# Optimization experiments

Hardware: AMD Instinct MI355X
Metric: run time of the kernel (lower is better)

The kernel has to match this reference:

```python
import jax, jax.numpy as jnp
import numpy as np

B, T, D, H, QK = 4, 2048, 1024, 16, 64
MAX_WAVELENGTH = 10000


def apply_rope(x, positions):
    # x: [B, T, H, d]; positions: [B, T] int
    d = x.shape[-1]
    fraction = 2 * jnp.arange(0, d // 2, dtype=jnp.int32) / d
    timescale = MAX_WAVELENGTH ** fraction  # [d/2]
    sinusoid = positions[..., None] / timescale[None, :]  # [B, T, d/2]
    sinusoid = sinusoid[..., None, :]  # [B, T, 1, d/2]
    sin, cos = jnp.sin(sinusoid), jnp.cos(sinusoid)
    x1, x2 = jnp.split(x, 2, axis=-1)
    return jnp.concatenate([x1 * cos - x2 * sin, x2 * cos + x1 * sin], axis=-1).astype(x.dtype)


def rms_norm(x, scale):
    var = jnp.mean(jnp.square(x), axis=-1, keepdims=True)
    return x * jax.lax.rsqrt(var + 1e-6) * (1 + scale)


def setup_inputs() -> dict:
    key = jax.random.key(0)
    ks = jax.random.split(key, 12)
    s = 0.02
    pos = jnp.broadcast_to(jnp.arange(T, dtype=jnp.int32), (B, T))
    causal = jnp.tril(jnp.ones((T, T), dtype=bool))[None, None]  # [1,1,T,T]
    return {
        "q": jax.random.normal(ks[0], (B, T, D), jnp.float32),
        "kv": jax.random.normal(ks[1], (B, T, D), jnp.float32),
        "mask": jnp.broadcast_to(causal, (B, 1, T, T)),
        "q_positions": pos,
        "kv_positions": pos,
        "Wq": jax.random.normal(ks[2], (D, H * QK), jnp.float32) * s,
        "bq": jnp.zeros((H * QK,), jnp.float32),
        "Wk": jax.random.normal(ks[3], (D, H * QK), jnp.float32) * s,
        "bk": jnp.zeros((H * QK,), jnp.float32),
        "Wv": jax.random.normal(ks[4], (D, H * QK), jnp.float32) * s,
        "bv": jnp.zeros((H * QK,), jnp.float32),
        "q_scale": jnp.zeros((QK,), jnp.float32),
        "k_scale": jnp.zeros((QK,), jnp.float32),
        "head_scale": jnp.zeros((1, H, 1), jnp.float32),
        "Wo": jax.random.normal(ks[5], (H * QK, D), jnp.float32) * s,
        "bo": jnp.zeros((D,), jnp.float32),
    }


def reference(q, kv, mask, q_positions, kv_positions, Wq, bq, Wk, bk, Wv, bv,
              q_scale, k_scale, head_scale, Wo, bo):
    qh = (q @ Wq + bq).reshape(B, T, H, QK)
    kh = (kv @ Wk + bk).reshape(B, T, H, QK)
    vh = (kv @ Wv + bv).reshape(B, T, H, QK)
    # qk layer norm (RMSNorm with (1+scale))
    qh = rms_norm(qh, q_scale)
    kh = rms_norm(kh, k_scale)
    # RoPE
    qh = apply_rope(qh, q_positions)
    kh = apply_rope(kh, kv_positions)
    # attention
    logits = jnp.einsum('bthd,bThd->bhtT', qh, kh) / np.sqrt(QK).astype(q.dtype)
    logits = jnp.where(mask, logits, jnp.finfo(logits.dtype).min)
    weights = jax.nn.softmax(logits, axis=-1)
    weights = jnp.where(mask, weights, 0)
    attn = jnp.einsum('bhtT,bThd->bthd', weights, vh)
    attn = attn * (1 + head_scale)  # [1,H,1] broadcasts over (t,h,d)
    return attn.reshape(B, T, H * QK) @ Wo + bo
```

## Files before the change

kernel.cpp:

```cpp
#include <hip/hip_runtime.h>
#include <math.h>

#define BB 4
#define TT 2048
#define DD 1024
#define HH 16
#define QKD 64
#define MM (BB*TT)
#define NN 1024
#define KK 1024

#define BKQ 32
#define NTS (KK/BKQ)

typedef unsigned short u16;
typedef __attribute__((ext_vector_type(8))) short short8;
typedef __attribute__((ext_vector_type(4))) float float4v;

__device__ __forceinline__ u16 f2bf(float f) {
    union { float f; unsigned u; } v; v.f = f;
    unsigned r = (v.u + 0x7FFFu + ((v.u >> 16) & 1u)) >> 16;
    return (u16)r;
}

__device__ __forceinline__ unsigned cvt_pk_bf16(float lo, float hi) {
    unsigned r;
    asm("v_cvt_pk_bf16_f32 %0, %1, %2" : "=v"(r) : "v"(lo), "v"(hi));
    return r;
}

typedef __attribute__((address_space(3))) unsigned lds_u32_t;
typedef __attribute__((address_space(1))) const unsigned glb_u32_t;
__device__ __forceinline__ void gl2lds16(const u16* g, u16* l) {
    __builtin_amdgcn_global_load_lds((glb_u32_t*)g, (lds_u32_t*)l, 16, 0, 0);
}

__global__ __launch_bounds__(256) void acast_kernel(
    const float* __restrict__ a, const float* __restrict__ b,
    u16* __restrict__ da, u16* __restrict__ db)
{
    const float* s = blockIdx.y ? b : a;
    u16* d = blockIdx.y ? db : da;
    size_t i = ((size_t)blockIdx.x * 256 + threadIdx.x) * 4;
    float4 v = *(const float4*)&s[i];
    ushort4 o = { f2bf(v.x), f2bf(v.y), f2bf(v.z), f2bf(v.w) };
    *(ushort4*)&d[i] = o;
}

__global__ __launch_bounds__(256) void wt_kernel(
    const float* __restrict__ Wq, const float* __restrict__ Wk,
    const float* __restrict__ Wv, const float* __restrict__ Wo,
    u16* __restrict__ dstbase)
{
    const int z = blockIdx.z;
    const float* src = (z == 0) ? Wq : (z == 1) ? Wk : (z == 2) ? Wv : Wo;
    u16* out = dstbase + (size_t)z * (KK * NN);
    const int bi = blockIdx.y, bj = blockIdx.x;
    __shared__ float tile[64][65];
    const int t = threadIdx.x;
    #pragma unroll
    for (int p = 0; p < 4; p++) {
        int idx = p * 256 + t;
        int r = idx >> 4, c4 = (idx & 15) << 2;
        float4 v = *(const float4*)&src[(size_t)(bi * 64 + r) * NN + bj * 64 + c4];
        tile[r][c4 + 0] = v.x; tile[r][c4 + 1] = v.y;
        tile[r][c4 + 2] = v.z; tile[r][c4 + 3] = v.w;
    }
    __syncthreads();
    #pragma unroll
    for (int p = 0; p < 4; p++) {
        int idx = p * 256 + t;
        int rn = idx >> 4, c4 = (idx & 15) << 2;
        ushort4 o = { f2bf(tile[c4 + 0][rn]), f2bf(tile[c4 + 1][rn]),
                      f2bf(tile[c4 + 2][rn]), f2bf(tile[c4 + 3][rn]) };
        *(ushort4*)&out[(size_t)(bj * 64 + rn) * KK + bi * 64 + c4] = o;
    }
}

__device__ __forceinline__ void gemm256_mainloop(
    const u16* __restrict__ A, const u16* __restrict__ Bt,
    int m0, int n0, u16* __restrict__ sh, float4v (&acc)[8][4])
{
    const int tid = threadIdx.x;
    const int lane = tid & 63;
    const int l15 = lane & 15, lg = lane >> 4;
    const int wave = tid >> 6;
    const int wm = wave >> 2, wn = wave & 3;

    u16* sA = sh;
    u16* sB = sh + 16384;

    const int c0 = tid, c1 = 512 + tid;
    const int r0s = c0 >> 2, g0 = (c0 & 3) ^ (r0s & 3);
    const int r1s = c1 >> 2, g1 = (c1 & 3) ^ (r1s & 3);

    const u16* gA0 = A  + (size_t)(m0 + r0s) * KK + g0 * 8;
    const u16* gA1 = A  + (size_t)(m0 + r1s) * KK + g1 * 8;
    const u16* gB0 = Bt + (size_t)(n0 + r0s) * KK + g0 * 8;
    const u16* gB1 = Bt + (size_t)(n0 + r1s) * KK + g1 * 8;

    auto issue = [&](int buf, int k0) {
        u16* dA = sA + buf * (256 * 32);
        u16* dB = sB + buf * (256 * 32);
        gl2lds16(gA0 + k0, dA + c0 * 8);
        gl2lds16(gA1 + k0, dA + c1 * 8);
        gl2lds16(gB0 + k0, dB + c0 * 8);
        gl2lds16(gB1 + k0, dB + c1 * 8);
    };

    issue(0, 0);
    issue(1, BKQ);
    asm volatile("s_waitcnt vmcnt(4)" ::: "memory");
    __builtin_amdgcn_s_barrier();
    __builtin_amdgcn_sched_barrier(0);

    for (int t = 0; t < NTS; t++) {
        const int buf = t & 1;
        const u16* cA = sA + buf * (256 * 32);
        const u16* cB = sB + buf * (256 * 32);

        short8 af[8], bf[4];
        #pragma unroll
        for (int x = 0; x < 8; x++) {
            int ra = wm * 128 + x * 16 + l15;
            af[x] = *(const short8*)(cA + (ra * 4 + (lg ^ (ra & 3))) * 8);
        }
        #pragma unroll
        for (int x = 0; x < 4; x++) {
            int rb = wn * 64 + x * 16 + l15;
            bf[x] = *(const short8*)(cB + (rb * 4 + (lg ^ (rb & 3))) * 8);
        }
        __builtin_amdgcn_s_setprio(1);
        #pragma unroll
        for (int mi = 0; mi < 8; mi++)
            #pragma unroll
            for (int nj = 0; nj < 4; nj++)
                acc[mi][nj] = __builtin_amdgcn_mfma_f32_16x16x32_bf16(af[mi], bf[nj], acc[mi][nj], 0, 0, 0);
        __builtin_amdgcn_s_setprio(0);

        __builtin_amdgcn_s_barrier();
        if (t + 2 < NTS) {
            issue(buf, (t + 2) * BKQ);
            asm volatile("s_waitcnt vmcnt(4)" ::: "memory");
        } else {
            asm volatile("s_waitcnt vmcnt(0)" ::: "memory");
        }
        __builtin_amdgcn_s_barrier();
        __builtin_amdgcn_sched_barrier(0);
    }
}

__device__ __forceinline__ void xcd_swizzle_4x32(int& m_idx, int& n_idx) {
    const int flat = blockIdx.y * 4 + blockIdx.x;
    const int xcd = flat & 7, q = flat >> 3;
    m_idx = xcd * 4 + (q & 3);
    n_idx = q >> 2;
}

__global__ __launch_bounds__(512) void qkv_gemm(
    const u16* __restrict__ qb, const u16* __restrict__ kvb,
    const u16* __restrict__ Wt,
    const float* __restrict__ bq, const float* __restrict__ bk, const float* __restrict__ bv,
    const int* __restrict__ qpos, const int* __restrict__ kpos,
    const float* __restrict__ q_scale, const float* __restrict__ k_scale,
    u16* __restrict__ qh, u16* __restrict__ kh, u16* __restrict__ vt)
{
    __shared__ __align__(16) u16 sh[32768];

    const int z = blockIdx.z;
    const u16* A        = (z == 0) ? qb : kvb;
    const u16* B        = Wt + (size_t)z * (KK * NN);
    const float* bias   = (z == 0) ? bq : (z == 1) ? bk : bv;
    const float* scl    = (z == 0) ? q_scale : k_scale;
    const int* pos_arr  = (z == 0) ? qpos : kpos;
    u16* dst            = (z == 0) ? qh : (z == 1) ? kh : vt;

    int m_idx, n_idx;
    xcd_swizzle_4x32(m_idx, n_idx);
    const int m0 = m_idx * 256, n0 = n_idx * 256;

    float4v acc[8][4];
    #pragma unroll
    for (int i = 0; i < 8; i++)
        #pragma unroll
        for (int j = 0; j < 4; j++) acc[i][j] = (float4v){0.f, 0.f, 0.f, 0.f};

    gemm256_mainloop(A, B, m0, n0, sh, acc);

    const int tid = threadIdx.x;
    const int lane = tid & 63, wave = tid >> 6;
    const int l15 = lane & 15, lg = lane >> 4;
    const int wm = wave >> 2, wn = wave & 3;

    float bia[4], sc[4];
    #pragma unroll
    for (int nj = 0; nj < 4; nj++) {
        bia[nj] = bias[n0 + wn * 64 + nj * 16 + l15];
        sc[nj]  = 1.0f + scl[nj * 16 + l15];
    }
    float invts[2];
    #pragma unroll
    for (int p = 0; p < 2; p++)
        invts[p] = powf(10000.0f, -(float)(p * 16 + l15) * (1.0f / 32.0f));

    const float QMUL = 0.125f * 1.44269504088896340736f;
    const int bb_ = m0 >> 11;
    const int t0g = m0 & 2047;

    if (z < 2) {
        #pragma unroll
        for (int p = 0; p < 2; p++) {
            __syncthreads();
            if (wm == p) {
                #pragma unroll
                for (int mi = 0; mi < 8; mi++) {
                    #pragma unroll
                    for (int r = 0; r < 4; r++) {
                        const int tl = mi * 16 + lg * 4 + r;
                        const int m = m0 + p * 128 + tl;
                        const int b = m >> 11, t = m & 2047;
                        float v[4];
                        #pragma unroll
                        for (int nj = 0; nj < 4; nj++) v[nj] = acc[mi][nj][r] + bia[nj];

                        float ss = v[0]*v[0] + v[1]*v[1] + v[2]*v[2] + v[3]*v[3];
                        ss += __shfl_xor(ss, 1);
                        ss += __shfl_xor(ss, 2);
                        ss += __shfl_xor(ss, 4);
                        ss += __shfl_xor(ss, 8);
                        float rn = rsqrtf(ss * (1.0f / 64.0f) + 1e-6f);
                        #pragma unroll
                        for (int nj = 0; nj < 4; nj++) v[nj] = v[nj] * rn * sc[nj];

                        const float pos = (float)pos_arr[b * TT + t];
                        #pragma unroll
                        for (int pp = 0; pp < 2; pp++) {
                            float ang = pos * invts[pp];
                            float s = sinf(ang), c = cosf(ang);
                            float x1 = v[pp], x2 = v[pp + 2];
                            v[pp]     = x1 * c - x2 * s;
                            v[pp + 2] = x2 * c + x1 * s;
                        }
                        if (z == 0) {
                            #pragma unroll
                            for (int nj = 0; nj < 4; nj++) v[nj] *= QMUL;
                        }
                        #pragma unroll
                        for (int nj = 0; nj < 4; nj++) {
                            const int dl = wn * 64 + nj * 16 + l15;
                            sh[tl * 256 + (dl ^ ((tl & 7) << 3))] = f2bf(v[nj]);
                        }
                    }
                }
            }
            __syncthreads();
            #pragma unroll
            for (int it = 0; it < 8; it++) {
                int idx = it * 512 + tid;
                int tl  = idx >> 5;
                int c8  = (idx & 31) << 3;
                short8 v8 = *(const short8*)&sh[tl * 256 + (c8 ^ ((tl & 7) << 3))];
                int cg = n0 + c8;
                int hh_ = cg >> 6, dih = cg & 63;
                int t = t0g + p * 128 + tl;
                *(short8*)&dst[((size_t)(bb_ * HH + hh_) * TT + t) * QKD + dih] = v8;
            }
        }
    } else {
        #pragma unroll
        for (int p = 0; p < 2; p++) {
            __syncthreads();
            if (wm == p) {
                #pragma unroll
                for (int mi = 0; mi < 8; mi++) {
                    #pragma unroll
                    for (int r = 0; r < 4; r++) {
                        const int tl = mi * 16 + lg * 4 + r;
                        #pragma unroll
                        for (int nj = 0; nj < 4; nj++) {
                            const int dl = wn * 64 + nj * 16 + l15;
                            sh[dl * 128 + (tl ^ ((dl & 7) << 3))] = f2bf(acc[mi][nj][r] + bia[nj]);
                        }
                    }
                }
            }
            __syncthreads();
            #pragma unroll
            for (int it = 0; it < 8; it++) {
                int idx = it * 512 + tid;
                int dl  = idx >> 4;
                int tc  = (idx & 15) << 3;
                short8 v8 = *(const short8*)&sh[dl * 128 + (tc ^ ((dl & 7) << 3))];
                int dg = n0 + dl;
                int hh_ = dg >> 6, dih = dg & 63;
                *(short8*)&vt[((size_t)(bb_ * HH + hh_) * QKD + dih) * TT + t0g + p * 128 + tc] = v8;
            }
        }
    }
}

__global__ __launch_bounds__(512) void out_gemm(
    const u16* __restrict__ A, const u16* __restrict__ Bt,
    const float* __restrict__ bo, float* __restrict__ out)
{
    __shared__ __align__(16) u16 sh[32768];

    int m_idx, n_idx;
    xcd_swizzle_4x32(m_idx, n_idx);
    const int m0 = m_idx * 256, n0 = n_idx * 256;

    float4v acc[8][4];
    #pragma unroll
    for (int i = 0; i < 8; i++)
        #pragma unroll
        for (int j = 0; j < 4; j++) acc[i][j] = (float4v){0.f, 0.f, 0.f, 0.f};

    gemm256_mainloop(A, Bt, m0, n0, sh, acc);

    const int lane = threadIdx.x & 63, wave = threadIdx.x >> 6;
    const int l15 = lane & 15, lg = lane >> 4;
    const int wm = wave >> 2, wn = wave & 3;

    float bov[4];
    #pragma unroll
    for (int nj = 0; nj < 4; nj++) bov[nj] = bo[n0 + wn * 64 + nj * 16 + l15];

    #pragma unroll
    for (int mi = 0; mi < 8; mi++)
        #pragma unroll
        for (int r = 0; r < 4; r++) {
            const int m = m0 + wm * 128 + mi * 16 + lg * 4 + r;
            float* op = out + (size_t)m * NN + n0 + wn * 64 + l15;
            #pragma unroll
            for (int nj = 0; nj < 4; nj++)
                op[nj * 16] = acc[mi][nj][r] + bov[nj];
        }
}

__global__ __launch_bounds__(256) void attn_mfma(
    const u16* __restrict__ qh, const u16* __restrict__ kh,
    const u16* __restrict__ vt, const float* __restrict__ head_scale,
    u16* __restrict__ out)
{
    __shared__ __align__(16) u16 Ks[2][64 * 64];
    __shared__ __align__(16) u16 Vs[2][64 * 64];
    __shared__ __align__(16) u16 Ps[4][16 * 64];

    const int b = blockIdx.z, h = blockIdx.y;
    const int qta = blockIdx.x;
    const int qtb = 31 - qta;
    const int t0a = qta * 64, t0b = qtb * 64;

    const int tid  = threadIdx.x;
    const int wave = tid >> 6, lane = tid & 63;
    const int l15 = lane & 15, lg = lane >> 4;
    const int l7 = l15 & 7;

    const size_t bh = (size_t)(b * HH + h);
    const u16* qbh  = qh + bh * TT * QKD;
    const u16* kbh  = kh + bh * TT * QKD;
    const u16* vtbh = vt + bh * QKD * TT;

    short8 qfA[2], qfB[2];
    #pragma unroll
    for (int kc = 0; kc < 2; kc++) {
        qfA[kc] = *(const short8*)(qbh + (size_t)(t0a + wave * 16 + l15) * QKD
                                    + kc * 32 + lg * 8);
        qfB[kc] = *(const short8*)(qbh + (size_t)(t0b + wave * 16 + l15) * QKD
                                    + kc * 32 + lg * 8);
    }

    auto stage = [&](int buf, int j0s) {
        #pragma unroll
        for (int rr = 0; rr < 2; rr++) {
            const int c   = rr * 256 + tid;
            const int row = c >> 3;
            const int g   = (c & 7) ^ (row & 7);
            u16* ldsK = &Ks[buf][(rr * 256 + (wave << 6)) * 8];
            u16* ldsV = &Vs[buf][(rr * 256 + (wave << 6)) * 8];
            gl2lds16(kbh  + (size_t)(j0s + row) * QKD + g * 8, ldsK);
            gl2lds16(vtbh + (size_t)row * TT + j0s + g * 8, ldsV);
        }
    };

    float4v oA[4], oB[4];
    #pragma unroll
    for (int nt = 0; nt < 4; nt++) {
        oA[nt] = (float4v){0.f, 0.f, 0.f, 0.f};
        oB[nt] = (float4v){0.f, 0.f, 0.f, 0.f};
    }
    float mA[4] = {-INFINITY, -INFINITY, -INFINITY, -INFINITY};
    float mB[4] = {-INFINITY, -INFINITY, -INFINITY, -INFINITY};
    float lA[4] = {0.f, 0.f, 0.f, 0.f};
    float lB[4] = {0.f, 0.f, 0.f, 0.f};

    auto flash_step = [&](int cur, int jt, int qt_self,
                          short8 (&qf)[2], float4v (&oa)[4],
                          float (&mr)[4], float (&lr)[4]) {
        float4v sarr[4];
        #pragma unroll
        for (int nt = 0; nt < 4; nt++) {
            float4v s = (float4v){0.f, 0.f, 0.f, 0.f};
            #pragma unroll
            for (int kc = 0; kc < 2; kc++) {
                const short8 bfrag = *(const short8*)
                    &Ks[cur][(nt * 16 + l15) * 64 + ((kc * 4 + lg) ^ l7) * 8];
                s = __builtin_amdgcn_mfma_f32_16x16x32_bf16(qf[kc], bfrag, s, 0, 0, 0);
            }
            sarr[nt] = s;
        }

        if (jt == qt_self) {
            const int qbase = qt_self * 64 + wave * 16 + lg * 4;
            #pragma unroll
            for (int nt = 0; nt < 4; nt++) {
                int jkey = jt * 64 + nt * 16 + l15;
                #pragma unroll
                for (int r = 0; r < 4; r++)
                    if (jkey > qbase + r) sarr[nt][r] = -INFINITY;
            }
        }

        float pm[4];
        #pragma unroll
        for (int r = 0; r < 4; r++) {
            float m = fmaxf(fmaxf(sarr[0][r], sarr[1][r]), fmaxf(sarr[2][r], sarr[3][r]));
            m = fmaxf(m, __shfl_xor(m, 1));
            m = fmaxf(m, __shfl_xor(m, 2));
            m = fmaxf(m, __shfl_xor(m, 4));
            m = fmaxf(m, __shfl_xor(m, 8));
            pm[r] = m;
        }
        float grow = fmaxf(fmaxf(pm[0] - mr[0], pm[1] - mr[1]),
                           fmaxf(pm[2] - mr[2], pm[3] - mr[3]));
        if (__any(grow > 8.0f)) {
            #pragma unroll
            for (int r = 0; r < 4; r++) {
                float mn = fmaxf(mr[r], pm[r]);
                float a  = exp2f(mr[r] - mn);
                mr[r] = mn;
                lr[r] *= a;
                #pragma unroll
                for (int nt = 0; nt < 4; nt++) oa[nt][r] *= a;
            }
        }

        u16* pw = Ps[wave];
        float lp[4] = {0.f, 0.f, 0.f, 0.f};
        #pragma unroll
        for (int nt = 0; nt < 4; nt++) {
            float p0 = exp2f(sarr[nt][0] - mr[0]);
            float p1 = exp2f(sarr[nt][1] - mr[1]);
            float p2 = exp2f(sarr[nt][2] - mr[2]);
            float p3 = exp2f(sarr[nt][3] - mr[3]);
            lp[0] += p0; lp[1] += p1; lp[2] += p2; lp[3] += p3;
            unsigned wlo = cvt_pk_bf16(p0, p1);
            unsigned whi = cvt_pk_bf16(p2, p3);
            const int gb = nt * 2 + (l15 >> 3);
            const int r0 = lg * 4;
            pw[(r0 + 0) * 64 + ((gb ^ ((r0 + 0) & 7))) * 8 + l7] = (u16)wlo;
            pw[(r0 + 1) * 64 + ((gb ^ ((r0 + 1) & 7))) * 8 + l7] = (u16)(wlo >> 16);
            pw[(r0 + 2) * 64 + ((gb ^ ((r0 + 2) & 7))) * 8 + l7] = (u16)whi;
            pw[(r0 + 3) * 64 + ((gb ^ ((r0 + 3) & 7))) * 8 + l7] = (u16)(whi >> 16);
        }
        #pragma unroll
        for (int r = 0; r < 4; r++) lr[r] += lp[r];

        short8 pf[2];
        #pragma unroll
        for (int kc = 0; kc < 2; kc++)
            pf[kc] = *(const short8*)&pw[l15 * 64 + ((kc * 4 + lg) ^ l7) * 8];

        #pragma unroll
        for (int nt = 0; nt < 4; nt++) {
            #pragma unroll
            for (int kc = 0; kc < 2; kc++) {
                const short8 vfrag = *(const short8*)
                    &Vs[cur][(nt * 16 + l15) * 64 + ((kc * 4 + lg) ^ l7) * 8];
                oa[nt] = __builtin_amdgcn_mfma_f32_16x16x32_bf16(pf[kc], vfrag, oa[nt], 0, 0, 0);
            }
        }
    };

    stage(0, 0);
    __syncthreads();

    const int njt = qtb + 1;
    for (int jt = 0; jt < njt; jt++) {
        const int cur = jt & 1;
        if (jt + 1 < njt) stage(cur ^ 1, (jt + 1) * 64);

        flash_step(cur, jt, qtb, qfB, oB, mB, lB);
        if (jt <= qta)
            flash_step(cur, jt, qta, qfA, oA, mA, lA);

        __syncthreads();
    }

    const float hs = 1.0f + head_scale[h];
    auto epilogue = [&](int t0, float4v (&oa)[4], float (&lr)[4]) {
        #pragma unroll
        for (int r = 0; r < 4; r++) {
            float l = lr[r];
            l += __shfl_xor(l, 1);
            l += __shfl_xor(l, 2);
            l += __shfl_xor(l, 4);
            l += __shfl_xor(l, 8);
            const int q = t0 + wave * 16 + lg * 4 + r;
            const float f = hs / l;
            u16* op = out + ((size_t)(b * TT + q) * NN) + h * QKD + l15;
            #pragma unroll
            for (int nt = 0; nt < 4; nt++)
                op[nt * 16] = f2bf(oa[nt][r] * f);
        }
    };
    epilogue(t0b, oB, lB);
    epilogue(t0a, oA, lA);
}

extern "C" void kernel_launch(void* const* d_in, const int* in_sizes, int n_in,
                              void* d_out, int out_size, void* d_ws, size_t ws_size,
                              hipStream_t stream)
{
    const float* q          = (const float*)d_in[0];
    const float* kv         = (const float*)d_in[1];
    const int*   qpos       = (const int*)d_in[3];
    const int*   kpos       = (const int*)d_in[4];
    const float* Wq         = (const float*)d_in[5];
    const float* bq         = (const float*)d_in[6];
    const float* Wk         = (const float*)d_in[7];
    const float* bk         = (const float*)d_in[8];
    const float* Wv         = (const float*)d_in[9];
    const float* bv         = (const float*)d_in[10];
    const float* q_scale    = (const float*)d_in[11];
    const float* k_scale    = (const float*)d_in[12];
    const float* head_scale = (const float*)d_in[13];
    const float* Wo         = (const float*)d_in[14];
    const float* bo         = (const float*)d_in[15];
    float* out = (float*)d_out;

    char* ws = (char*)d_ws;
    u16* qb     = (u16*)(ws);
    u16* kvb    = (u16*)(ws + (16u << 20));
    u16* Wt     = (u16*)(ws + (32u << 20));
    u16* qh_b   = (u16*)(ws + (40u << 20));
    u16* kh_b   = (u16*)(ws + (56u << 20));
    u16* vt_b   = (u16*)(ws + (72u << 20));
    u16* attn_b = (u16*)(ws + (88u << 20));

    acast_kernel<<<dim3(MM * DD / (256 * 4), 2), 256, 0, stream>>>(q, kv, qb, kvb);
    wt_kernel<<<dim3(16, 16, 4), 256, 0, stream>>>(Wq, Wk, Wv, Wo, Wt);
    qkv_gemm<<<dim3(NN / 256, MM / 256, 3), 512, 0, stream>>>(
        qb, kvb, Wt, bq, bk, bv, qpos, kpos, q_scale, k_scale, qh_b, kh_b, vt_b);
    attn_mfma<<<dim3(TT / 128, HH, BB), 256, 0, stream>>>(qh_b, kh_b, vt_b, head_scale, attn_b);
    out_gemm<<<dim3(NN / 256, MM / 256), 512, 0, stream>>>(attn_b, Wt + (size_t)3 * KK * NN, bo, out);
}
```

Before: 487.8 us.

## Triple-buffer GEMM main loop with split A-fragment loads and new LDS swizzle

Turns the shared 256x256 GEMM main loop from double to triple buffering: three K-tiles are prefetched and each iteration needs only one barrier pair, with graded vmcnt waits. A-fragment LDS reads are split into two halves interleaved with MFMA groups, and the XOR swizzle now uses (row>>1)&3 to change the bank-conflict pattern. LDS per block grows to 96 KB and launch bounds request 2 blocks per CU, which may raise register pressure or prevent two blocks from co-residing. The aim is to hide global-load latency and LDS-read stalls in both QKV and output projections.

```diff
diff --git a/kernel.cpp b/kernel.cpp
--- a/kernel.cpp
+++ b/kernel.cpp
@@ -87,12 +87,9 @@
     const int wave = tid >> 6;
     const int wm = wave >> 2, wn = wave & 3;
 
-    u16* sA = sh;
-    u16* sB = sh + 16384;
-
     const int c0 = tid, c1 = 512 + tid;
-    const int r0s = c0 >> 2, g0 = (c0 & 3) ^ (r0s & 3);
-    const int r1s = c1 >> 2, g1 = (c1 & 3) ^ (r1s & 3);
+    const int r0s = c0 >> 2, g0 = (c0 & 3) ^ ((r0s >> 1) & 3);
+    const int r1s = c1 >> 2, g1 = (c1 & 3) ^ ((r1s >> 1) & 3);
 
     const u16* gA0 = A  + (size_t)(m0 + r0s) * KK + g0 * 8;
     const u16* gA1 = A  + (size_t)(m0 + r1s) * KK + g1 * 8;
@@ -100,8 +97,8 @@
     const u16* gB1 = Bt + (size_t)(n0 + r1s) * KK + g1 * 8;
 
     auto issue = [&](int buf, int k0) {
-        u16* dA = sA + buf * (256 * 32);
-        u16* dB = sB + buf * (256 * 32);
+        u16* dA = sh + buf * 16384;
+        u16* dB = dA + 8192;
         gl2lds16(gA0 + k0, dA + c0 * 8);
         gl2lds16(gA1 + k0, dA + c1 * 8);
         gl2lds16(gB0 + k0, dB + c0 * 8);
@@ -110,42 +107,55 @@
 
     issue(0, 0);
     issue(1, BKQ);
-    asm volatile("s_waitcnt vmcnt(4)" ::: "memory");
-    __builtin_amdgcn_s_barrier();
-    __builtin_amdgcn_sched_barrier(0);
-
+    issue(2, 2 * BKQ);
+
+    int buf = 0;
     for (int t = 0; t < NTS; t++) {
-        const int buf = t & 1;
-        const u16* cA = sA + buf * (256 * 32);
-        const u16* cB = sB + buf * (256 * 32);
-
-        short8 af[8], bf[4];
-        #pragma unroll
-        for (int x = 0; x < 8; x++) {
-            int ra = wm * 128 + x * 16 + l15;
-            af[x] = *(const short8*)(cA + (ra * 4 + (lg ^ (ra & 3))) * 8);
-        }
+        if (t < NTS - 2)       asm volatile("s_waitcnt vmcnt(8)" ::: "memory");
+        else if (t == NTS - 2) asm volatile("s_waitcnt vmcnt(4)" ::: "memory");
+        else                   asm volatile("s_waitcnt vmcnt(0)" ::: "memory");
+        __builtin_amdgcn_s_barrier();
+        __builtin_amdgcn_sched_barrier(0);
+
+        const u16* cA = sh + buf * 16384;
+        const u16* cB = cA + 8192;
+
+        short8 bf[4];
         #pragma unroll
         for (int x = 0; x < 4; x++) {
             int rb = wn * 64 + x * 16 + l15;
-            bf[x] = *(const short8*)(cB + (rb * 4 + (lg ^ (rb & 3))) * 8);
+            bf[x] = *(const short8*)(cB + (rb * 4 + (lg ^ ((rb >> 1) & 3))) * 8);
+        }
+        short8 afl[4];
+        #pragma unroll
+        for (int x = 0; x < 4; x++) {
+            int ra = wm * 128 + x * 16 + l15;
+            afl[x] = *(const short8*)(cA + (ra * 4 + (lg ^ ((ra >> 1) & 3))) * 8);
         }
         __builtin_amdgcn_s_setprio(1);
         #pragma unroll
-        for (int mi = 0; mi < 8; mi++)
+        for (int mi = 0; mi < 4; mi++)
             #pragma unroll
             for (int nj = 0; nj < 4; nj++)
-                acc[mi][nj] = __builtin_amdgcn_mfma_f32_16x16x32_bf16(af[mi], bf[nj], acc[mi][nj], 0, 0, 0);
+                acc[mi][nj] = __builtin_amdgcn_mfma_f32_16x16x32_bf16(afl[mi], bf[nj], acc[mi][nj], 0, 0, 0);
         __builtin_amdgcn_s_setprio(0);
+        short8 afh[4];
+        #pragma unroll
+        for (int x = 0; x < 4; x++) {
+            int ra = wm * 128 + (4 + x) * 16 + l15;
+            afh[x] = *(const short8*)(cA + (ra * 4 + (lg ^ ((ra >> 1) & 3))) * 8);
+        }
+        __builtin_amdgcn_s_setprio(1);
+        #pragma unroll
+        for (int mi = 0; mi < 4; mi++)
+            #pragma unroll
+            for (int nj = 0; nj < 4; nj++)
+                acc[4 + mi][nj] = __builtin_amdgcn_mfma_f32_16x16x32_bf16(afh[mi], bf[nj], acc[4 + mi][nj], 0, 0, 0);
+        __builtin_amdgcn_s_setprio(0);
 
         __builtin_amdgcn_s_barrier();
-        if (t + 2 < NTS) {
-            issue(buf, (t + 2) * BKQ);
-            asm volatile("s_waitcnt vmcnt(4)" ::: "memory");
-        } else {
-            asm volatile("s_waitcnt vmcnt(0)" ::: "memory");
-        }
-        __builtin_amdgcn_s_barrier();
+        if (t + 3 < NTS) issue(buf, (t + 3) * BKQ);
+        buf = (buf == 2) ? 0 : buf + 1;
         __builtin_amdgcn_sched_barrier(0);
     }
 }
@@ -157,7 +167,7 @@
     n_idx = q >> 2;
 }
 
-__global__ __launch_bounds__(512) void qkv_gemm(
+__global__ __launch_bounds__(512, 2) void qkv_gemm(
     const u16* __restrict__ qb, const u16* __restrict__ kvb,
     const u16* __restrict__ Wt,
     const float* __restrict__ bq, const float* __restrict__ bk, const float* __restrict__ bv,
@@ -165,7 +175,7 @@
     const float* __restrict__ q_scale, const float* __restrict__ k_scale,
     u16* __restrict__ qh, u16* __restrict__ kh, u16* __restrict__ vt)
 {
-    __shared__ __align__(16) u16 sh[32768];
+    __shared__ __align__(16) u16 sh[49152];
 
     const int z = blockIdx.z;
     const u16* A        = (z == 0) ? qb : kvb;
@@ -299,11 +309,11 @@
     }
 }
 
-__global__ __launch_bounds__(512) void out_gemm(
+__global__ __launch_bounds__(512, 2) void out_gemm(
     const u16* __restrict__ A, const u16* __restrict__ Bt,
     const float* __restrict__ bo, float* __restrict__ out)
 {
-    __shared__ __align__(16) u16 sh[32768];
+    __shared__ __align__(16) u16 sh[49152];
 
     int m_idx, n_idx;
     xcd_swizzle_4x32(m_idx, n_idx);
```

Result: no change. 482.3 us (-1.1%).

## Deepen GEMM K-tile to 64 with new LDS swizzle and restructured double buffering

Applied to the files above, without the earlier changes.

The shared 256x256 GEMM mainloop now loads 64-wide K tiles (16 iterations instead of 32). It uses a 3-bit XOR swizzle over eight 16-byte slots per row and a simpler issue-next-then-compute double-buffer loop. LDS per block doubles to 128 KB, and launch bounds request 2 blocks per CU. The aim is to halve barrier and wait overhead per unit of MFMA work. The larger LDS footprint may limit occupancy, and prefetch distance drops from two tiles ahead to one.

```diff
diff --git a/kernel.cpp b/kernel.cpp
--- a/kernel.cpp
+++ b/kernel.cpp
@@ -10,8 +10,8 @@
 #define NN 1024
 #define KK 1024
 
-#define BKQ 32
-#define NTS (KK/BKQ)
+#define BKG 64
+#define NTSG (KK/BKG)
 
 typedef unsigned short u16;
 typedef __attribute__((ext_vector_type(8))) short short8;
@@ -33,6 +33,11 @@
 typedef __attribute__((address_space(1))) const unsigned glb_u32_t;
 __device__ __forceinline__ void gl2lds16(const u16* g, u16* l) {
     __builtin_amdgcn_global_load_lds((glb_u32_t*)g, (lds_u32_t*)l, 16, 0, 0);
+}
+
+__device__ __forceinline__ int swz_slot(int row, int slot) {
+    const int j = (row >> 2) & 3;
+    return slot ^ ((j & 1) | ((j & 2) * 3));
 }
 
 __global__ __launch_bounds__(256) void acast_kernel(
@@ -87,64 +92,64 @@
     const int wave = tid >> 6;
     const int wm = wave >> 2, wn = wave & 3;
 
-    u16* sA = sh;
-    u16* sB = sh + 16384;
-
-    const int c0 = tid, c1 = 512 + tid;
-    const int r0s = c0 >> 2, g0 = (c0 & 3) ^ (r0s & 3);
-    const int r1s = c1 >> 2, g1 = (c1 & 3) ^ (r1s & 3);
-
-    const u16* gA0 = A  + (size_t)(m0 + r0s) * KK + g0 * 8;
-    const u16* gA1 = A  + (size_t)(m0 + r1s) * KK + g1 * 8;
-    const u16* gB0 = Bt + (size_t)(n0 + r0s) * KK + g0 * 8;
-    const u16* gB1 = Bt + (size_t)(n0 + r1s) * KK + g1 * 8;
+    const u16* gA[4]; const u16* gB[4]; int ld_off[4];
+    #pragma unroll
+    for (int i = 0; i < 4; i++) {
+        const int c = tid + i * 512;
+        const int r = c >> 3, sp = c & 7;
+        const int gs = swz_slot(r, sp);
+        gA[i] = A  + (size_t)(m0 + r) * KK + gs * 8;
+        gB[i] = Bt + (size_t)(n0 + r) * KK + gs * 8;
+        ld_off[i] = c * 8;
+    }
 
     auto issue = [&](int buf, int k0) {
-        u16* dA = sA + buf * (256 * 32);
-        u16* dB = sB + buf * (256 * 32);
-        gl2lds16(gA0 + k0, dA + c0 * 8);
-        gl2lds16(gA1 + k0, dA + c1 * 8);
-        gl2lds16(gB0 + k0, dB + c0 * 8);
-        gl2lds16(gB1 + k0, dB + c1 * 8);
+        u16* dA = sh + buf * 32768;
+        u16* dB = dA + 16384;
+        #pragma unroll
+        for (int i = 0; i < 4; i++) gl2lds16(gA[i] + k0, dA + ld_off[i]);
+        #pragma unroll
+        for (int i = 0; i < 4; i++) gl2lds16(gB[i] + k0, dB + ld_off[i]);
     };
 
     issue(0, 0);
-    issue(1, BKQ);
-    asm volatile("s_waitcnt vmcnt(4)" ::: "memory");
-    __builtin_amdgcn_s_barrier();
-    __builtin_amdgcn_sched_barrier(0);
-
-    for (int t = 0; t < NTS; t++) {
+
+    for (int t = 0; t < NTSG; t++) {
         const int buf = t & 1;
-        const u16* cA = sA + buf * (256 * 32);
-        const u16* cB = sB + buf * (256 * 32);
-
-        short8 af[8], bf[4];
-        #pragma unroll
-        for (int x = 0; x < 8; x++) {
-            int ra = wm * 128 + x * 16 + l15;
-            af[x] = *(const short8*)(cA + (ra * 4 + (lg ^ (ra & 3))) * 8);
-        }
-        #pragma unroll
-        for (int x = 0; x < 4; x++) {
-            int rb = wn * 64 + x * 16 + l15;
-            bf[x] = *(const short8*)(cB + (rb * 4 + (lg ^ (rb & 3))) * 8);
-        }
-        __builtin_amdgcn_s_setprio(1);
-        #pragma unroll
-        for (int mi = 0; mi < 8; mi++)
-            #pragma unroll
-            for (int nj = 0; nj < 4; nj++)
-                acc[mi][nj] = __builtin_amdgcn_mfma_f32_16x16x32_bf16(af[mi], bf[nj], acc[mi][nj], 0, 0, 0);
-        __builtin_amdgcn_s_setprio(0);
-
-        __builtin_amdgcn_s_barrier();
-        if (t + 2 < NTS) {
-            issue(buf, (t + 2) * BKQ);
-            asm volatile("s_waitcnt vmcnt(4)" ::: "memory");
+        if (t + 1 < NTSG) {
+            issue(buf ^ 1, (t + 1) * BKG);
+            asm volatile("s_waitcnt vmcnt(8)" ::: "memory");
         } else {
             asm volatile("s_waitcnt vmcnt(0)" ::: "memory");
         }
+        __builtin_amdgcn_s_barrier();
+        __builtin_amdgcn_sched_barrier(0);
+
+        const u16* cA = sh + buf * 32768;
+        const u16* cB = cA + 16384;
+
+        #pragma unroll
+        for (int kk = 0; kk < 2; kk++) {
+            short8 af[8], bf[4];
+            #pragma unroll
+            for (int x = 0; x < 8; x++) {
+                const int ra = wm * 128 + x * 16 + l15;
+                af[x] = *(const short8*)(cA + ra * 64 + swz_slot(ra, kk * 4 + lg) * 8);
+            }
+            #pragma unroll
+            for (int x = 0; x < 4; x++) {
+                const int rb = wn * 64 + x * 16 + l15;
+                bf[x] = *(const short8*)(cB + rb * 64 + swz_slot(rb, kk * 4 + lg) * 8);
+            }
+            __builtin_amdgcn_s_setprio(1);
+            #pragma unroll
+            for (int mi = 0; mi < 8; mi++)
+                #pragma unroll
+                for (int nj = 0; nj < 4; nj++)
+                    acc[mi][nj] = __builtin_amdgcn_mfma_f32_16x16x32_bf16(af[mi], bf[nj], acc[mi][nj], 0, 0, 0);
+            __builtin_amdgcn_s_setprio(0);
+        }
+
         __builtin_amdgcn_s_barrier();
         __builtin_amdgcn_sched_barrier(0);
     }
@@ -157,7 +162,7 @@
     n_idx = q >> 2;
 }
 
-__global__ __launch_bounds__(512) void qkv_gemm(
+__global__ __launch_bounds__(512, 2) void qkv_gemm(
     const u16* __restrict__ qb, const u16* __restrict__ kvb,
     const u16* __restrict__ Wt,
     const float* __restrict__ bq, const float* __restrict__ bk, const float* __restrict__ bv,
@@ -165,7 +170,7 @@
     const float* __restrict__ q_scale, const float* __restrict__ k_scale,
     u16* __restrict__ qh, u16* __restrict__ kh, u16* __restrict__ vt)
 {
-    __shared__ __align__(16) u16 sh[32768];
+    __shared__ __align__(16) u16 sh[65536];
 
     const int z = blockIdx.z;
     const u16* A        = (z == 0) ? qb : kvb;
@@ -299,11 +304,11 @@
     }
 }
 
-__global__ __launch_bounds__(512) void out_gemm(
+__global__ __launch_bounds__(512, 2) void out_gemm(
     const u16* __restrict__ A, const u16* __restrict__ Bt,
     const float* __restrict__ bo, float* __restrict__ out)
 {
-    __shared__ __align__(16) u16 sh[32768];
+    __shared__ __align__(16) u16 sh[65536];
 
     int m_idx, n_idx;
     xcd_swizzle_4x32(m_idx, n_idx);
```

Result: slower. 500.5 us (+2.6%).
